# Kernel optimization log

Hardware: AMD Instinct MI355X
Metric: run time of the kernel (lower is better)

Reference implementation:

```python
import jax, jax.numpy as jnp
import numpy as np

B, A = 4096, 8          # episodes, agents per episode
N = B * A               # total nodes
E = B * A * (A - 1)     # fully-connected directed edges within each group
F_IN, D, H, M, NA = 64, 64, 4, 64, 10  # in_feat, gnn_dim, heads, mem_dim, n_actions
NEG_SLOPE = 0.2
LN_EPS = 1e-5


def _build_edge_index():
    base = np.arange(A)
    s = np.repeat(base, A)
    d = np.tile(base, A)
    keep = s != d
    s, d = s[keep], d[keep]                       # [A*(A-1)]
    offs = (np.arange(B) * A)[:, None]
    src = (offs + s[None, :]).reshape(-1)
    dst = (offs + d[None, :]).reshape(-1)
    return jnp.asarray(np.stack([src, dst]), dtype=jnp.int32)  # [2, E]


def setup_inputs() -> dict:
    key = jax.random.key(0)
    ks = jax.random.split(key, 16)
    sc = 0.05
    return {
        "x": jax.random.normal(ks[0], (N, F_IN), jnp.float32),
        "edge_attr": jax.random.normal(ks[1], (E, 3), jnp.float32),
        "hidden": jax.random.normal(ks[2], (N, M), jnp.float32) * sc,
        "edge_index": _build_edge_index(),
        # GATv2 params
        "Wl": jax.random.normal(ks[3], (H * D, F_IN), jnp.float32) * sc,
        "bl": jnp.zeros((H * D,), jnp.float32),
        "Wr": jax.random.normal(ks[4], (H * D, F_IN), jnp.float32) * sc,
        "br": jnp.zeros((H * D,), jnp.float32),
        "We": jax.random.normal(ks[5], (H * D, 3), jnp.float32) * sc,
        "be": jnp.zeros((H * D,), jnp.float32),
        "att": jax.random.normal(ks[6], (H, D), jnp.float32) * sc,
        "bias_g": jnp.zeros((D,), jnp.float32),
        # GRUCell params (gate order r,z,n as in torch)
        "W_ih": jax.random.normal(ks[7], (3 * M, D), jnp.float32) * sc,
        "W_hh": jax.random.normal(ks[8], (3 * M, M), jnp.float32) * sc,
        "b_ih": jnp.zeros((3 * M,), jnp.float32),
        "b_hh": jnp.zeros((3 * M,), jnp.float32),
        # LayerNorm + output Linear
        "ln_g": jnp.ones((M,), jnp.float32),
        "ln_b": jnp.zeros((M,), jnp.float32),
        "Wq": jax.random.normal(ks[9], (NA, M), jnp.float32) * sc,
        "bq": jnp.zeros((NA,), jnp.float32),
    }


def reference(x, edge_attr, hidden, edge_index, Wl, bl, Wr, br, We, be, att,
              bias_g, W_ih, W_hh, b_ih, b_hh, ln_g, ln_b, Wq, bq):
    src, dst = edge_index[0], edge_index[1]
    # GATv2Conv (concat=False -> mean over heads), share_weights=False
    xl = (x @ Wl.T + bl).reshape(N, H, D)          # source projection
    xr = (x @ Wr.T + br).reshape(N, H, D)          # target projection
    ee = (edge_attr @ We.T + be).reshape(E, H, D)  # edge embedding
    m = jax.nn.leaky_relu(xl[src] + xr[dst] + ee, NEG_SLOPE)  # [E,H,D]
    logits = jnp.einsum('ehd,hd->eh', m, att)                  # [E,H]
    lmax = jax.ops.segment_max(logits, dst, num_segments=N)    # [N,H]
    ex = jnp.exp(logits - lmax[dst])
    denom = jax.ops.segment_sum(ex, dst, num_segments=N)       # [N,H]
    alpha = ex / denom[dst]                                    # softmax per target
    agg = jax.ops.segment_sum(alpha[:, :, None] * xl[src], dst, num_segments=N)  # [N,H,D]
    h_gnn = jax.nn.relu(agg.mean(axis=1) + bias_g)             # [N,D]
    # GRUCell
    gi = h_gnn @ W_ih.T + b_ih
    gh = hidden @ W_hh.T + b_hh
    ir, iz, inn = jnp.split(gi, 3, axis=-1)
    hr, hz, hn = jnp.split(gh, 3, axis=-1)
    r = jax.nn.sigmoid(ir + hr)
    z = jax.nn.sigmoid(iz + hz)
    n = jnp.tanh(inn + r * hn)
    h = (1.0 - z) * n + z * hidden                              # [N,M]
    # LayerNorm + Linear head
    mu = h.mean(axis=-1, keepdims=True)
    var = ((h - mu) ** 2).mean(axis=-1, keepdims=True)
    hln = (h - mu) / jnp.sqrt(var + LN_EPS) * ln_g + ln_b
    q = hln @ Wq.T + bq                                         # [N,NA]
    return q, h
```

## Files before the change

### kernel.cpp

```cpp
#include <hip/hip_runtime.h>

typedef unsigned short u16;
typedef unsigned int u32;
typedef __attribute__((ext_vector_type(8))) short bf16x8;
typedef __attribute__((ext_vector_type(4))) float f32x4;
typedef _Float16 f16;
typedef __attribute__((ext_vector_type(2))) f16 h2;
typedef __attribute__((ext_vector_type(8))) f16 h8;

#define NAG 8
#define NAGB 16
#define FIN 64
#define MDIM 64
#define NACT 10
#define EPG 56
#define NTOT 32768
#define ABP 72
#define XLS 296
#define XHS 72

#define U_XR  4736
#define U_RZ  0
#define U_HNH 4224
#define U_INB 5312
#define U_HG  6400
#define U_LNH 6400

#define WQOFF 57344

__device__ __forceinline__ float b2f(u16 u) {
  return __uint_as_float(((unsigned int)u) << 16);
}
__device__ __forceinline__ u16 f2b(float f) {
  unsigned int x = __float_as_uint(f);
  unsigned int r = x + 0x7fffu + ((x >> 16) & 1u);
  return (u16)(r >> 16);
}
__device__ __forceinline__ u16 f2h(float f) {
  f16 h = (f16)f; u16 u; __builtin_memcpy(&u, &h, 2); return u;
}
__device__ __forceinline__ float h2f(u16 u) {
  f16 h; __builtin_memcpy(&h, &u, 2); return (float)h;
}
__device__ __forceinline__ u32 pkh2(float a, float b) {
#if __has_builtin(__builtin_amdgcn_cvt_pkrtz)
  auto r = __builtin_amdgcn_cvt_pkrtz(a, b);
  u32 u; __builtin_memcpy(&u, &r, 4); return u;
#else
  return (u32)f2h(a) | ((u32)f2h(b) << 16);
#endif
}

union H8u { h8 v; h2 p[4]; };

__device__ __forceinline__ h8 lrelu8(h8 m) {
  h8 s = m * (f16)0.2f;
#if __has_builtin(__builtin_elementwise_max)
  return __builtin_elementwise_max(m, s);
#else
  h8 r;
#pragma unroll
  for (int i = 0; i < 8; i++) r[i] = (m[i] > s[i]) ? m[i] : s[i];
  return r;
#endif
}

#if __has_builtin(__builtin_amdgcn_fdot2)
__device__ __forceinline__ float dotacc(h2 a, h2 b, float c) {
  return __builtin_amdgcn_fdot2(a, b, c, false);
}
#else
__device__ __forceinline__ float dotacc(h2 a, h2 b, float c) {
  c += (float)a[0] * (float)b[0];
  c += (float)a[1] * (float)b[1];
  return c;
}
#endif

__global__ __launch_bounds__(256) void prep_weights(
    const float* __restrict__ Wl, const float* __restrict__ Wr,
    const float* __restrict__ Wih, const float* __restrict__ Whh,
    const float* __restrict__ Wq,
    u16* __restrict__ wsB)
{
  const int idx = blockIdx.x * 256 + threadIdx.x;
  if (idx >= 57 * 2 * 64) return;
  const int L  = idx & 63;
  const int ks = (idx >> 6) & 1;
  const int T  = idx >> 7;
  u16 v[8];
  if (T < 56) {
    const float* W; int row0;
    if      (T < 16) { W = Wl;  row0 = T * 16; }
    else if (T < 32) { W = Wr;  row0 = (T - 16) * 16; }
    else if (T < 44) { W = Wih; row0 = (T - 32) * 16; }
    else             { W = Whh; row0 = (T - 44) * 16; }
    const int row = row0 + (L & 15);
    const int k0  = ks * 32 + (L >> 4) * 8;
#pragma unroll
    for (int j = 0; j < 8; j++) v[j] = f2b(W[row * 64 + k0 + j]);
  } else {
    const int row = L & 15;
    const int k0  = ks * 32 + (L >> 4) * 8;
#pragma unroll
    for (int j = 0; j < 8; j++)
      v[j] = (row < NACT) ? f2h(Wq[row * 64 + k0 + j]) : (u16)0;
  }
  *(bf16x8*)(wsB + (size_t)idx * 8) = *(bf16x8*)v;
}

__global__ __launch_bounds__(256, 6) void gnn_rnn_kernel(
    const float* __restrict__ x, const float* __restrict__ edge_attr,
    const float* __restrict__ hidden,
    const float* __restrict__ bl, const float* __restrict__ br,
    const float* __restrict__ We, const float* __restrict__ be,
    const float* __restrict__ att, const float* __restrict__ bias_g,
    const float* __restrict__ b_ih, const float* __restrict__ b_hh,
    const float* __restrict__ ln_g, const float* __restrict__ ln_b,
    const float* __restrict__ Wq, const float* __restrict__ bq,
    const u16* __restrict__ wsB,
    float* __restrict__ d_out)
{
  __shared__ __align__(16) char uraw[18944];
  __shared__ __align__(16) u16 s_xb[NAGB * ABP];
  __shared__ __align__(16) u16 s_al[NAGB * 4 * 8];
  __shared__ __align__(16) u16 s_hidb[NAGB * ABP];
  __shared__ __align__(16) u16 s_w0h[256], s_w1h[256], s_w2h[256], s_atth[256];

  u16*   uXL  = (u16*)uraw;
  u16*   uXR  = (u16*)uraw + U_XR;
  u16*   uHn  = (u16*)uraw + U_HNH;
  u16*   uInn = (u16*)uraw + U_INB;
  u16*   s_hgb = (u16*)uraw + U_HG;
  u16*   uLnH = (u16*)uraw + U_LNH;
  float* uF   = (float*)uraw;

  const int t = threadIdx.x;
  const int b = blockIdx.x;
  const int L = t & 63;
  const int w = t >> 6;
  const int q = L >> 4;

  {
    const float4 xv = ((const float4*)(x + b * (NAGB * FIN)))[t];
    const float4 hv = ((const float4*)(hidden + b * (NAGB * MDIM)))[t];
    const int a = (t * 4) >> 6, m = (t * 4) & 63;
    u16 px[4] = { f2b(xv.x), f2b(xv.y), f2b(xv.z), f2b(xv.w) };
    u16 ph[4] = { f2b(hv.x), f2b(hv.y), f2b(hv.z), f2b(hv.w) };
    *(uint2*)&s_xb[a * ABP + m]   = *(uint2*)px;
    *(uint2*)&s_hidb[a * ABP + m] = *(uint2*)ph;
    s_w0h[t]  = f2h(We[t * 3]);
    s_w1h[t]  = f2h(We[t * 3 + 1]);
    s_w2h[t]  = f2h(We[t * 3 + 2]);
    s_atth[t] = f2h(att[t]);
  }
  float ea00 = 0.f, ea01 = 0.f, ea02 = 0.f, ea10 = 0.f, ea11 = 0.f, ea12 = 0.f;
  if (L < EPG) {
    const float* eb = edge_attr + b * (2 * EPG * 3) + L * 3;
    ea00 = eb[0]; ea01 = eb[1]; ea02 = eb[2];
    ea10 = eb[EPG * 3]; ea11 = eb[EPG * 3 + 1]; ea12 = eb[EPG * 3 + 2];
  }
  __syncthreads();

  {
    const int arow = L & 15;
    bf16x8 af0 = *(const bf16x8*)&s_xb[arow * ABP + q * 8];
    bf16x8 af1 = *(const bf16x8*)&s_xb[arow * ABP + 32 + q * 8];
    const bf16x8* wsBv = (const bf16x8*)wsB;
#pragma unroll 4
    for (int i = 0; i < 8; i++) {
      const int T = w * 8 + i;
      f32x4 acc = {0.f, 0.f, 0.f, 0.f};
      acc = __builtin_amdgcn_mfma_f32_16x16x32_bf16(wsBv[(T * 2 + 0) * 64 + L], af0, acc, 0, 0, 0);
      acc = __builtin_amdgcn_mfma_f32_16x16x32_bf16(wsBv[(T * 2 + 1) * 64 + L], af1, acc, 0, 0, 0);
      const int agent = L & 15;
      const int Tm = T & 15;
      const int h = Tm >> 2;
      const int gcb = Tm * 16 + q * 4;
      const int d0 = (Tm & 3) * 16 + q * 4;
      f32x4 bias4;
      if (T < 16) bias4 = *(const f32x4*)(bl + gcb);
      else        bias4 = *(const f32x4*)(br + gcb) + *(const f32x4*)(be + gcb);
      f32x4 v = acc + bias4;
      u32 pk2[2] = { pkh2(v[0], v[1]), pkh2(v[2], v[3]) };
      u16* dst = (T < 16 ? uXL : uXR) + agent * XLS + h * XHS + d0;
      *(uint2*)dst = *(uint2*)pk2;
    }
  }
  __syncthreads();

  {
    const int h = w;
    if (L < EPG) {
      const int e = L;
      const int s = e / 7, k = e % 7;
      const int j = k + (k >= s ? 1 : 0);
      const f16 a00 = (f16)ea00, a01 = (f16)ea01, a02 = (f16)ea02;
      const f16 a10 = (f16)ea10, a11 = (f16)ea11, a12 = (f16)ea12;
      const u16* xlp0 = uXL + s * XLS + h * XHS;
      const u16* xrp0 = uXR + j * XLS + h * XHS;
      const u16* xlp1 = uXL + (8 + s) * XLS + h * XHS;
      const u16* xrp1 = uXR + (8 + j) * XLS + h * XHS;
      const u16* w0p = s_w0h + h * 64;
      const u16* w1p = s_w1h + h * 64;
      const u16* w2p = s_w2h + h * 64;
      const u16* atp = s_atth + h * 64;
      float lgA0 = 0.f, lgB0 = 0.f, lgA1 = 0.f, lgB1 = 0.f;
#pragma unroll 2
      for (int kq = 0; kq < 8; kq++) {
        H8u w0, w1, w2, at, x0, r0, x1, r1, m0, m1;
        w0.v = *(const h8*)(w0p + kq * 8);
        w1.v = *(const h8*)(w1p + kq * 8);
        w2.v = *(const h8*)(w2p + kq * 8);
        at.v = *(const h8*)(atp + kq * 8);
        x0.v = *(const h8*)(xlp0 + kq * 8);
        r0.v = *(const h8*)(xrp0 + kq * 8);
        x1.v = *(const h8*)(xlp1 + kq * 8);
        r1.v = *(const h8*)(xrp1 + kq * 8);
        m0.v = x0.v + r0.v + w0.v * a00 + w1.v * a01 + w2.v * a02;
        m0.v = lrelu8(m0.v);
        m1.v = x1.v + r1.v + w0.v * a10 + w1.v * a11 + w2.v * a12;
        m1.v = lrelu8(m1.v);
        lgA0 = dotacc(m0.p[0], at.p[0], lgA0);
        lgB0 = dotacc(m0.p[1], at.p[1], lgB0);
        lgA0 = dotacc(m0.p[2], at.p[2], lgA0);
        lgB0 = dotacc(m0.p[3], at.p[3], lgB0);
        lgA1 = dotacc(m1.p[0], at.p[0], lgA1);
        lgB1 = dotacc(m1.p[1], at.p[1], lgB1);
        lgA1 = dotacc(m1.p[2], at.p[2], lgA1);
        lgB1 = dotacc(m1.p[3], at.p[3], lgB1);
      }
      s_al[((    j) * 4 + h) * 8 + s] = f2h(__expf(lgA0 + lgB0));
      s_al[((8 + j) * 4 + h) * 8 + s] = f2h(__expf(lgA1 + lgB1));
    } else {
      const int j2 = L - EPG;
      s_al[((    j2) * 4 + w) * 8 + j2] = 0;
      s_al[((8 + j2) * 4 + w) * 8 + j2] = 0;
    }
  }
  __syncthreads();

  {
    const int ep = t >> 7, jj = (t >> 4) & 7, dq = t & 15;
    const int a16 = ep * 8 + jj;
    float acc[4] = {0.f, 0.f, 0.f, 0.f};
#pragma unroll
    for (int h = 0; h < 4; h++) {
      H8u av;
      av.v = *(const h8*)&s_al[(a16 * 4 + h) * 8];
      h2 d2 = (av.p[0] + av.p[1]) + (av.p[2] + av.p[3]);
      float den = (float)d2[0] + (float)d2[1];
      h2 ah0 = {(f16)0.f, (f16)0.f};
      h2 ah1 = {(f16)0.f, (f16)0.f};
#pragma unroll
      for (int s = 0; s < 8; s++) {
        const u16* xp = uXL + (ep * 8 + s) * XLS + h * XHS + dq * 4;
        uint2 xv = *(const uint2*)xp;
        h2 x01, x23;
        __builtin_memcpy(&x01, &xv.x, 4);
        __builtin_memcpy(&x23, &xv.y, 4);
        f16 al = av.v[s];
        h2 al2 = {al, al};
        ah0 += al2 * x01;
        ah1 += al2 * x23;
      }
      const float inv = 1.f / den;
      acc[0] += (float)ah0[0] * inv;
      acc[1] += (float)ah0[1] * inv;
      acc[2] += (float)ah1[0] * inv;
      acc[3] += (float)ah1[1] * inv;
    }
    const f32x4 bg = *(const f32x4*)(bias_g + dq * 4);
    u16 pk[4];
#pragma unroll
    for (int c = 0; c < 4; c++) {
      float v = acc[c] * 0.25f + bg[c];
      pk[c] = f2b(v > 0.f ? v : 0.f);
    }
    *(uint2*)&s_hgb[a16 * ABP + dq * 4] = *(uint2*)pk;
  }
  __syncthreads();

  {
    const int arow = L & 15;
    bf16x8 ag0 = *(const bf16x8*)&s_hgb[arow * ABP + q * 8];
    bf16x8 ag1 = *(const bf16x8*)&s_hgb[arow * ABP + 32 + q * 8];
    bf16x8 ah0 = *(const bf16x8*)&s_hidb[arow * ABP + q * 8];
    bf16x8 ah1 = *(const bf16x8*)&s_hidb[arow * ABP + 32 + q * 8];
    const bf16x8* wsBv = (const bf16x8*)wsB;
#pragma unroll
    for (int i = 0; i < 3; i++) {
      const int T6 = w * 3 + i;
      const int Tg = 32 + T6, Th = 44 + T6;
      f32x4 acci = {0.f, 0.f, 0.f, 0.f};
      acci = __builtin_amdgcn_mfma_f32_16x16x32_bf16(wsBv[(Tg * 2 + 0) * 64 + L], ag0, acci, 0, 0, 0);
      acci = __builtin_amdgcn_mfma_f32_16x16x32_bf16(wsBv[(Tg * 2 + 1) * 64 + L], ag1, acci, 0, 0, 0);
      f32x4 acch = {0.f, 0.f, 0.f, 0.f};
      acch = __builtin_amdgcn_mfma_f32_16x16x32_bf16(wsBv[(Th * 2 + 0) * 64 + L], ah0, acch, 0, 0, 0);
      acch = __builtin_amdgcn_mfma_f32_16x16x32_bf16(wsBv[(Th * 2 + 1) * 64 + L], ah1, acch, 0, 0, 0);
      const int agent = L & 15;
      const int gcb = T6 * 16 + q * 4;
      if (T6 < 8) {
        f32x4 bsum = *(const f32x4*)(b_ih + gcb) + *(const f32x4*)(b_hh + gcb);
        f32x4 v = acci + acch + bsum;
        *(f32x4*)&uF[U_RZ + agent * 132 + gcb] = v;
      } else {
        f32x4 vi = acci + *(const f32x4*)(b_ih + gcb);
        f32x4 vh = acch + *(const f32x4*)(b_hh + gcb);
        const int off = agent * 68 + (gcb - 128);
        u32 pi[2] = { pkh2(vi[0], vi[1]), pkh2(vi[2], vi[3]) };
        u32 ph[2] = { pkh2(vh[0], vh[1]), pkh2(vh[2], vh[3]) };
        *(uint2*)&uInn[off] = *(uint2*)pi;
        *(uint2*)&uHn[off]  = *(uint2*)ph;
      }
    }
  }
  __syncthreads();

  {
    const float lng = ln_g[L];
    const float lnb = ln_b[L];
#pragma unroll
    for (int rr = 0; rr < 4; rr++) {
      const int a = w + rr * 4, m = L;
      float rz_r = uF[U_RZ + a * 132 + m];
      float rz_z = uF[U_RZ + a * 132 + 64 + m];
      float inn  = h2f(uInn[a * 68 + m]);
      float hn   = h2f(uHn[a * 68 + m]);
      float hid  = b2f(s_hidb[a * ABP + m]);
      float r = 1.f / (1.f + __expf(-rz_r));
      float z = 1.f / (1.f + __expf(-rz_z));
      float xg = inn + r * hn;
      xg = fminf(fmaxf(xg, -20.f), 20.f);
      float e2 = __expf(2.f * xg);
      float n = (e2 - 1.f) / (e2 + 1.f);
      float hv = (1.f - z) * n + z * hid;
      d_out[NTOT * NACT + (b * NAGB + a) * MDIM + m] = hv;
      float sum = hv, sq = hv * hv;
#pragma unroll
      for (int off = 1; off < 64; off <<= 1) {
        sum += __shfl_xor(sum, off, 64);
        sq  += __shfl_xor(sq,  off, 64);
      }
      float mu  = sum * (1.f / 64.f);
      float var = sq * (1.f / 64.f) - mu * mu;
      var = var > 0.f ? var : 0.f;
      uLnH[a * ABP + m] = f2h((hv - mu) * rsqrtf(var + 1e-5f) * lng + lnb);
    }
  }
  __syncthreads();

  if (w == 0) {
    const int agent = L & 15;
    const u16* wq = wsB + WQOFF;
    h8 wq0, wq1, ln0, ln1;
    wq0 = *(const h8*)(wq + (size_t)(0 * 64 + L) * 8);
    wq1 = *(const h8*)(wq + (size_t)(1 * 64 + L) * 8);
    ln0 = *(const h8*)(uLnH + agent * ABP + q * 8);
    ln1 = *(const h8*)(uLnH + agent * ABP + 32 + q * 8);
    f32x4 acc = {0.f, 0.f, 0.f, 0.f};
    acc = __builtin_amdgcn_mfma_f32_16x16x32_f16(wq0, ln0, acc, 0, 0, 0);
    acc = __builtin_amdgcn_mfma_f32_16x16x32_f16(wq1, ln1, acc, 0, 0, 0);
    float* qout = d_out + ((size_t)b * NAGB + agent) * NACT;
#pragma unroll
    for (int r = 0; r < 4; r++) {
      const int o = q * 4 + r;
      if (o < NACT) qout[o] = acc[r] + bq[o];
    }
  }
}

extern "C" void kernel_launch(void* const* d_in, const int* in_sizes, int n_in,
                              void* d_out, int out_size, void* d_ws, size_t ws_size,
                              hipStream_t stream) {
  const int N  = in_sizes[0] / FIN;
  const int Bn = N / NAGB;
  u16* wsB = (u16*)d_ws;

  prep_weights<<<29, 256, 0, stream>>>(
      (const float*)d_in[4],
      (const float*)d_in[6],
      (const float*)d_in[12],
      (const float*)d_in[13],
      (const float*)d_in[18],
      wsB);

  gnn_rnn_kernel<<<Bn, 256, 0, stream>>>(
      (const float*)d_in[0], (const float*)d_in[1], (const float*)d_in[2],
      (const float*)d_in[5],
      (const float*)d_in[7],
      (const float*)d_in[8],
      (const float*)d_in[9],
      (const float*)d_in[10],
      (const float*)d_in[11],
      (const float*)d_in[14],
      (const float*)d_in[15],
      (const float*)d_in[16], (const float*)d_in[17],
      (const float*)d_in[18], (const float*)d_in[19],
      wsB, (float*)d_out);
}
```

Before: 136.7 us.

## Double block size to 512 threads and split per-block work across eight waves

Raises the workgroup from 256 to 512 threads and re-partitions every stage (input staging, MFMA projection tiles, per-edge logits, aggregation, GRU gate tiles, LayerNorm rows) so each wave does half the previous work. The aim is shorter per-block latency and more parallelism between the barriers for this small per-block problem. In exchange there are more waves per block to synchronise, some waves sit idle in the GRU stage (T6<12 guard), and register budget and occupancy change with the new launch bounds.

```diff
diff --git a/kernel.cpp b/kernel.cpp
--- a/kernel.cpp
+++ b/kernel.cpp
@@ -109,7 +109,7 @@
   *(bf16x8*)(wsB + (size_t)idx * 8) = *(bf16x8*)v;
 }
 
-__global__ __launch_bounds__(256, 6) void gnn_rnn_kernel(
+__global__ __launch_bounds__(512, 8) void gnn_rnn_kernel(
     const float* __restrict__ x, const float* __restrict__ edge_attr,
     const float* __restrict__ hidden,
     const float* __restrict__ bl, const float* __restrict__ br,
@@ -142,23 +142,25 @@
   const int q = L >> 4;
 
   {
-    const float4 xv = ((const float4*)(x + b * (NAGB * FIN)))[t];
-    const float4 hv = ((const float4*)(hidden + b * (NAGB * MDIM)))[t];
-    const int a = (t * 4) >> 6, m = (t * 4) & 63;
-    u16 px[4] = { f2b(xv.x), f2b(xv.y), f2b(xv.z), f2b(xv.w) };
-    u16 ph[4] = { f2b(hv.x), f2b(hv.y), f2b(hv.z), f2b(hv.w) };
-    *(uint2*)&s_xb[a * ABP + m]   = *(uint2*)px;
-    *(uint2*)&s_hidb[a * ABP + m] = *(uint2*)ph;
-    s_w0h[t]  = f2h(We[t * 3]);
-    s_w1h[t]  = f2h(We[t * 3 + 1]);
-    s_w2h[t]  = f2h(We[t * 3 + 2]);
-    s_atth[t] = f2h(att[t]);
-  }
-  float ea00 = 0.f, ea01 = 0.f, ea02 = 0.f, ea10 = 0.f, ea11 = 0.f, ea12 = 0.f;
+    const float2 xv = ((const float2*)(x + b * (NAGB * FIN)))[t];
+    const float2 hv = ((const float2*)(hidden + b * (NAGB * MDIM)))[t];
+    const int a = (t * 2) >> 6, m = (t * 2) & 63;
+    u16 px[2] = { f2b(xv.x), f2b(xv.y) };
+    u16 ph[2] = { f2b(hv.x), f2b(hv.y) };
+    *(u32*)&s_xb[a * ABP + m]   = *(u32*)px;
+    *(u32*)&s_hidb[a * ABP + m] = *(u32*)ph;
+    if (t < 256) {
+      s_w0h[t]  = f2h(We[t * 3]);
+      s_w1h[t]  = f2h(We[t * 3 + 1]);
+      s_w2h[t]  = f2h(We[t * 3 + 2]);
+      s_atth[t] = f2h(att[t]);
+    }
+  }
+  const int h3 = w >> 1, ep3 = w & 1;
+  float ea0 = 0.f, ea1 = 0.f, ea2 = 0.f;
   if (L < EPG) {
-    const float* eb = edge_attr + b * (2 * EPG * 3) + L * 3;
-    ea00 = eb[0]; ea01 = eb[1]; ea02 = eb[2];
-    ea10 = eb[EPG * 3]; ea11 = eb[EPG * 3 + 1]; ea12 = eb[EPG * 3 + 2];
+    const float* eb = edge_attr + b * (2 * EPG * 3) + ep3 * (EPG * 3) + L * 3;
+    ea0 = eb[0]; ea1 = eb[1]; ea2 = eb[2];
   }
   __syncthreads();
 
@@ -167,9 +169,9 @@
     bf16x8 af0 = *(const bf16x8*)&s_xb[arow * ABP + q * 8];
     bf16x8 af1 = *(const bf16x8*)&s_xb[arow * ABP + 32 + q * 8];
     const bf16x8* wsBv = (const bf16x8*)wsB;
-#pragma unroll 4
-    for (int i = 0; i < 8; i++) {
-      const int T = w * 8 + i;
+#pragma unroll
+    for (int i = 0; i < 4; i++) {
+      const int T = w * 4 + i;
       f32x4 acc = {0.f, 0.f, 0.f, 0.f};
       acc = __builtin_amdgcn_mfma_f32_16x16x32_bf16(wsBv[(T * 2 + 0) * 64 + L], af0, acc, 0, 0, 0);
       acc = __builtin_amdgcn_mfma_f32_16x16x32_bf16(wsBv[(T * 2 + 1) * 64 + L], af1, acc, 0, 0, 0);
@@ -190,94 +192,72 @@
   __syncthreads();
 
   {
-    const int h = w;
     if (L < EPG) {
       const int e = L;
       const int s = e / 7, k = e % 7;
       const int j = k + (k >= s ? 1 : 0);
-      const f16 a00 = (f16)ea00, a01 = (f16)ea01, a02 = (f16)ea02;
-      const f16 a10 = (f16)ea10, a11 = (f16)ea11, a12 = (f16)ea12;
-      const u16* xlp0 = uXL + s * XLS + h * XHS;
-      const u16* xrp0 = uXR + j * XLS + h * XHS;
-      const u16* xlp1 = uXL + (8 + s) * XLS + h * XHS;
-      const u16* xrp1 = uXR + (8 + j) * XLS + h * XHS;
-      const u16* w0p = s_w0h + h * 64;
-      const u16* w1p = s_w1h + h * 64;
-      const u16* w2p = s_w2h + h * 64;
-      const u16* atp = s_atth + h * 64;
-      float lgA0 = 0.f, lgB0 = 0.f, lgA1 = 0.f, lgB1 = 0.f;
+      const f16 a00 = (f16)ea0, a01 = (f16)ea1, a02 = (f16)ea2;
+      const u16* xlp = uXL + (ep3 * 8 + s) * XLS + h3 * XHS;
+      const u16* xrp = uXR + (ep3 * 8 + j) * XLS + h3 * XHS;
+      const u16* w0p = s_w0h + h3 * 64;
+      const u16* w1p = s_w1h + h3 * 64;
+      const u16* w2p = s_w2h + h3 * 64;
+      const u16* atp = s_atth + h3 * 64;
+      float lgA = 0.f, lgB = 0.f;
 #pragma unroll 2
       for (int kq = 0; kq < 8; kq++) {
-        H8u w0, w1, w2, at, x0, r0, x1, r1, m0, m1;
+        H8u w0, w1, w2, at, x0, r0, m0;
         w0.v = *(const h8*)(w0p + kq * 8);
         w1.v = *(const h8*)(w1p + kq * 8);
         w2.v = *(const h8*)(w2p + kq * 8);
         at.v = *(const h8*)(atp + kq * 8);
-        x0.v = *(const h8*)(xlp0 + kq * 8);
-        r0.v = *(const h8*)(xrp0 + kq * 8);
-        x1.v = *(const h8*)(xlp1 + kq * 8);
-        r1.v = *(const h8*)(xrp1 + kq * 8);
+        x0.v = *(const h8*)(xlp + kq * 8);
+        r0.v = *(const h8*)(xrp + kq * 8);
         m0.v = x0.v + r0.v + w0.v * a00 + w1.v * a01 + w2.v * a02;
         m0.v = lrelu8(m0.v);
-        m1.v = x1.v + r1.v + w0.v * a10 + w1.v * a11 + w2.v * a12;
-        m1.v = lrelu8(m1.v);
-        lgA0 = dotacc(m0.p[0], at.p[0], lgA0);
-        lgB0 = dotacc(m0.p[1], at.p[1], lgB0);
-        lgA0 = dotacc(m0.p[2], at.p[2], lgA0);
-        lgB0 = dotacc(m0.p[3], at.p[3], lgB0);
-        lgA1 = dotacc(m1.p[0], at.p[0], lgA1);
-        lgB1 = dotacc(m1.p[1], at.p[1], lgB1);
-        lgA1 = dotacc(m1.p[2], at.p[2], lgA1);
-        lgB1 = dotacc(m1.p[3], at.p[3], lgB1);
+        lgA = dotacc(m0.p[0], at.p[0], lgA);
+        lgB = dotacc(m0.p[1], at.p[1], lgB);
+        lgA = dotacc(m0.p[2], at.p[2], lgA);
+        lgB = dotacc(m0.p[3], at.p[3], lgB);
       }
-      s_al[((    j) * 4 + h) * 8 + s] = f2h(__expf(lgA0 + lgB0));
-      s_al[((8 + j) * 4 + h) * 8 + s] = f2h(__expf(lgA1 + lgB1));
+      s_al[((ep3 * 8 + j) * 4 + h3) * 8 + s] = f2h(__expf(lgA + lgB));
     } else {
       const int j2 = L - EPG;
-      s_al[((    j2) * 4 + w) * 8 + j2] = 0;
-      s_al[((8 + j2) * 4 + w) * 8 + j2] = 0;
-    }
-  }
-  __syncthreads();
-
-  {
-    const int ep = t >> 7, jj = (t >> 4) & 7, dq = t & 15;
+      s_al[((ep3 * 8 + j2) * 4 + h3) * 8 + j2] = 0;
+    }
+  }
+  __syncthreads();
+
+  {
+    const int ep = t >> 8, jj = (t >> 5) & 7, dq2 = t & 31;
     const int a16 = ep * 8 + jj;
-    float acc[4] = {0.f, 0.f, 0.f, 0.f};
+    float acc0 = 0.f, acc1 = 0.f;
 #pragma unroll
     for (int h = 0; h < 4; h++) {
       H8u av;
       av.v = *(const h8*)&s_al[(a16 * 4 + h) * 8];
       h2 d2 = (av.p[0] + av.p[1]) + (av.p[2] + av.p[3]);
       float den = (float)d2[0] + (float)d2[1];
-      h2 ah0 = {(f16)0.f, (f16)0.f};
-      h2 ah1 = {(f16)0.f, (f16)0.f};
+      h2 ah = {(f16)0.f, (f16)0.f};
 #pragma unroll
       for (int s = 0; s < 8; s++) {
-        const u16* xp = uXL + (ep * 8 + s) * XLS + h * XHS + dq * 4;
-        uint2 xv = *(const uint2*)xp;
-        h2 x01, x23;
-        __builtin_memcpy(&x01, &xv.x, 4);
-        __builtin_memcpy(&x23, &xv.y, 4);
+        const u16* xp = uXL + (ep * 8 + s) * XLS + h * XHS + dq2 * 2;
+        u32 xv = *(const u32*)xp;
+        h2 x01;
+        __builtin_memcpy(&x01, &xv, 4);
         f16 al = av.v[s];
         h2 al2 = {al, al};
-        ah0 += al2 * x01;
-        ah1 += al2 * x23;
+        ah += al2 * x01;
       }
       const float inv = 1.f / den;
-      acc[0] += (float)ah0[0] * inv;
-      acc[1] += (float)ah0[1] * inv;
-      acc[2] += (float)ah1[0] * inv;
-      acc[3] += (float)ah1[1] * inv;
-    }
-    const f32x4 bg = *(const f32x4*)(bias_g + dq * 4);
-    u16 pk[4];
-#pragma unroll
-    for (int c = 0; c < 4; c++) {
-      float v = acc[c] * 0.25f + bg[c];
-      pk[c] = f2b(v > 0.f ? v : 0.f);
-    }
-    *(uint2*)&s_hgb[a16 * ABP + dq * 4] = *(uint2*)pk;
+      acc0 += (float)ah[0] * inv;
+      acc1 += (float)ah[1] * inv;
+    }
+    const float2 bg = *(const float2*)(bias_g + dq2 * 2);
+    float v0 = acc0 * 0.25f + bg.x;
+    float v1 = acc1 * 0.25f + bg.y;
+    u16 pk[2] = { f2b(v0 > 0.f ? v0 : 0.f), f2b(v1 > 0.f ? v1 : 0.f) };
+    *(u32*)&s_hgb[a16 * ABP + dq2 * 2] = *(u32*)pk;
   }
   __syncthreads();
 
@@ -289,29 +269,31 @@
     bf16x8 ah1 = *(const bf16x8*)&s_hidb[arow * ABP + 32 + q * 8];
     const bf16x8* wsBv = (const bf16x8*)wsB;
 #pragma unroll
-    for (int i = 0; i < 3; i++) {
-      const int T6 = w * 3 + i;
-      const int Tg = 32 + T6, Th = 44 + T6;
-      f32x4 acci = {0.f, 0.f, 0.f, 0.f};
-      acci = __builtin_amdgcn_mfma_f32_16x16x32_bf16(wsBv[(Tg * 2 + 0) * 64 + L], ag0, acci, 0, 0, 0);
-      acci = __builtin_amdgcn_mfma_f32_16x16x32_bf16(wsBv[(Tg * 2 + 1) * 64 + L], ag1, acci, 0, 0, 0);
-      f32x4 acch = {0.f, 0.f, 0.f, 0.f};
-      acch = __builtin_amdgcn_mfma_f32_16x16x32_bf16(wsBv[(Th * 2 + 0) * 64 + L], ah0, acch, 0, 0, 0);
-      acch = __builtin_amdgcn_mfma_f32_16x16x32_bf16(wsBv[(Th * 2 + 1) * 64 + L], ah1, acch, 0, 0, 0);
-      const int agent = L & 15;
-      const int gcb = T6 * 16 + q * 4;
-      if (T6 < 8) {
-        f32x4 bsum = *(const f32x4*)(b_ih + gcb) + *(const f32x4*)(b_hh + gcb);
-        f32x4 v = acci + acch + bsum;
-        *(f32x4*)&uF[U_RZ + agent * 132 + gcb] = v;
-      } else {
-        f32x4 vi = acci + *(const f32x4*)(b_ih + gcb);
-        f32x4 vh = acch + *(const f32x4*)(b_hh + gcb);
-        const int off = agent * 68 + (gcb - 128);
-        u32 pi[2] = { pkh2(vi[0], vi[1]), pkh2(vi[2], vi[3]) };
-        u32 ph[2] = { pkh2(vh[0], vh[1]), pkh2(vh[2], vh[3]) };
-        *(uint2*)&uInn[off] = *(uint2*)pi;
-        *(uint2*)&uHn[off]  = *(uint2*)ph;
+    for (int i = 0; i < 2; i++) {
+      const int T6 = w * 2 + i;
+      if (T6 < 12) {
+        const int Tg = 32 + T6, Th = 44 + T6;
+        f32x4 acci = {0.f, 0.f, 0.f, 0.f};
+        acci = __builtin_amdgcn_mfma_f32_16x16x32_bf16(wsBv[(Tg * 2 + 0) * 64 + L], ag0, acci, 0, 0, 0);
+        acci = __builtin_amdgcn_mfma_f32_16x16x32_bf16(wsBv[(Tg * 2 + 1) * 64 + L], ag1, acci, 0, 0, 0);
+        f32x4 acch = {0.f, 0.f, 0.f, 0.f};
+        acch = __builtin_amdgcn_mfma_f32_16x16x32_bf16(wsBv[(Th * 2 + 0) * 64 + L], ah0, acch, 0, 0, 0);
+        acch = __builtin_amdgcn_mfma_f32_16x16x32_bf16(wsBv[(Th * 2 + 1) * 64 + L], ah1, acch, 0, 0, 0);
+        const int agent = L & 15;
+        const int gcb = T6 * 16 + q * 4;
+        if (T6 < 8) {
+          f32x4 bsum = *(const f32x4*)(b_ih + gcb) + *(const f32x4*)(b_hh + gcb);
+          f32x4 v = acci + acch + bsum;
+          *(f32x4*)&uF[U_RZ + agent * 132 + gcb] = v;
+        } else {
+          f32x4 vi = acci + *(const f32x4*)(b_ih + gcb);
+          f32x4 vh = acch + *(const f32x4*)(b_hh + gcb);
+          const int off = agent * 68 + (gcb - 128);
+          u32 pi[2] = { pkh2(vi[0], vi[1]), pkh2(vi[2], vi[3]) };
+          u32 ph[2] = { pkh2(vh[0], vh[1]), pkh2(vh[2], vh[3]) };
+          *(uint2*)&uInn[off] = *(uint2*)pi;
+          *(uint2*)&uHn[off]  = *(uint2*)ph;
+        }
       }
     }
   }
@@ -321,8 +303,8 @@
     const float lng = ln_g[L];
     const float lnb = ln_b[L];
 #pragma unroll
-    for (int rr = 0; rr < 4; rr++) {
-      const int a = w + rr * 4, m = L;
+    for (int rr = 0; rr < 2; rr++) {
+      const int a = w + rr * 8, m = L;
       float rz_r = uF[U_RZ + a * 132 + m];
       float rz_z = uF[U_RZ + a * 132 + 64 + m];
       float inn  = h2f(uInn[a * 68 + m]);
@@ -385,7 +367,7 @@
       (const float*)d_in[18],
       wsB);
 
-  gnn_rnn_kernel<<<Bn, 256, 0, stream>>>(
+  gnn_rnn_kernel<<<Bn, 512, 0, stream>>>(
       (const float*)d_in[0], (const float*)d_in[1], (const float*)d_in[2],
       (const float*)d_in[5],
       (const float*)d_in[7],
```

Result: no change. 136.0 us (-0.5%).
